# Kernel tuning notes

Measured on AMD Instinct MI355X. Metric: run time of the kernel, lower is better.

Reference implementation:

```python
import jax, jax.numpy as jnp
import numpy as np

N = 20000
E = 80000
D = 1024


def setup_inputs() -> dict:
    key = jax.random.key(0)
    ks = jax.random.split(key, 12)
    s1 = 1.0 / np.sqrt(2 * D)
    s2 = 1.0 / np.sqrt(D)
    return {
        "x": jax.random.normal(ks[0], (N, D), dtype=jnp.float32),
        "edge_index": jax.random.randint(ks[1], (2, E), 0, N, dtype=jnp.int64),
        "edge_attr": jax.random.normal(ks[2], (E, D), dtype=jnp.float32),
        "W1a": jax.random.uniform(ks[3], (2 * D, D), jnp.float32, -s1, s1),
        "b1a": jax.random.uniform(ks[4], (D,), jnp.float32, -s1, s1),
        "W1b": jax.random.uniform(ks[5], (D, D), jnp.float32, -s2, s2),
        "b1b": jax.random.uniform(ks[6], (D,), jnp.float32, -s2, s2),
        "W2a": jax.random.uniform(ks[7], (2 * D, D), jnp.float32, -s1, s1),
        "b2a": jax.random.uniform(ks[8], (D,), jnp.float32, -s1, s1),
        "W2b": jax.random.uniform(ks[9], (D, D), jnp.float32, -s2, s2),
        "b2b": jax.random.uniform(ks[10], (D,), jnp.float32, -s2, s2),
    }


def reference(x, edge_index, edge_attr, W1a, b1a, W1b, b1b, W2a, b2a, W2b, b2b):
    row, col = edge_index[0], edge_index[1]
    # gather source node features, concat edge features: [E, 2D]
    h = jnp.concatenate([x[row], edge_attr], axis=1)
    # node_mlp_1: Lin(2D,D) -> ReLU -> Lin(D,D)
    h = jax.nn.relu(h @ W1a + b1a) @ W1b + b1b  # [E, D]
    # scatter_mean over destination nodes (dim_size = N); empty segments -> 0
    sums = jax.ops.segment_sum(h, col, num_segments=N)  # [N, D]
    counts = jax.ops.segment_sum(jnp.ones((h.shape[0], 1), h.dtype), col, num_segments=N)
    mean = sums / jnp.maximum(counts, 1.0)
    # (scatter_max is computed in the torch code but its result is unused)
    out = jnp.concatenate([x, mean], axis=1)  # [N, 2D]
    # node_mlp_2
    return jax.nn.relu(out @ W2a + b2a) @ W2b + b2b  # [N, D]
```

## Files before the change

kernel.cpp:

```cpp
#include <hip/hip_runtime.h>
#include <stdint.h>

#define NN 20000
#define NE 80000
#define DD 1024

typedef __bf16 bf16x8 __attribute__((ext_vector_type(8)));
typedef float f32x4 __attribute__((ext_vector_type(4)));
typedef unsigned short u16;
typedef unsigned int u32;

__device__ __forceinline__ float bf2f(u16 v) { return __uint_as_float(((u32)v) << 16); }
__device__ __forceinline__ u16 f2bf(float f) { return (u16)((__float_as_uint(f) + 0x8000u) >> 16); }

__device__ __forceinline__ void lds_dma16(const u16* g, u16* l) {
  __builtin_amdgcn_global_load_lds((const __attribute__((address_space(1))) u32*)g,
                                   (__attribute__((address_space(3))) u32*)l, 16, 0, 0);
}

__global__ void detect_stride_k(const int* __restrict__ ei, int* flag) {
  if (threadIdx.x == 0) {
    int nz = 0;
    for (int i = 1; i < 128; i += 2) nz |= ei[i];
    *flag = (nz == 0) ? 2 : 1;
  }
}

__global__ void transpose_cvt_k(const float* __restrict__ in, u16* __restrict__ out) {
  __shared__ float tile[32][33];
  int bx = blockIdx.x * 32, by = blockIdx.y * 32;
  int tx = threadIdx.x & 31, ty = threadIdx.x >> 5;
#pragma unroll
  for (int s = 0; s < 4; s++)
    tile[ty + s * 8][tx] = in[(size_t)(by + ty + s * 8) * DD + bx + tx];
  __syncthreads();
#pragma unroll
  for (int s = 0; s < 4; s++)
    out[(size_t)(bx + ty + s * 8) * DD + by + tx] = f2bf(tile[tx][ty + s * 8]);
}

__global__ void cvt_bf16_k(const float4* __restrict__ in, ushort4* __restrict__ out, int n4) {
  int i = blockIdx.x * 256 + threadIdx.x;
  if (i < n4) {
    float4 f = in[i];
    ushort4 o;
    o.x = f2bf(f.x); o.y = f2bf(f.y); o.z = f2bf(f.z); o.w = f2bf(f.w);
    out[i] = o;
  }
}

__global__ void count_edges_k(const int* __restrict__ ei, const int* __restrict__ sflag,
                              int* __restrict__ cnt) {
  int e = blockIdx.x * 256 + threadIdx.x;
  if (e < NE) {
    int s = *sflag;
    atomicAdd(&cnt[ei[(size_t)s * (NE + e)]], 1);
  }
}

__global__ __launch_bounds__(1024) void scan_k(const int* __restrict__ cnt,
                                               int* __restrict__ rowptr, int* __restrict__ ofs) {
  __shared__ int part[1024];
  int t = threadIdx.x;
  int base = t * 20;
  int loc[20];
  int s = 0;
#pragma unroll
  for (int i = 0; i < 20; i++) {
    int v = (base + i < NN) ? cnt[base + i] : 0;
    loc[i] = s; s += v;
  }
  part[t] = s;
  __syncthreads();
  for (int d = 1; d < 1024; d <<= 1) {
    int v = (t >= d) ? part[t - d] : 0;
    __syncthreads();
    part[t] += v;
    __syncthreads();
  }
  int excl = (t > 0) ? part[t - 1] : 0;
#pragma unroll
  for (int i = 0; i < 20; i++)
    if (base + i < NN) { rowptr[base + i] = excl + loc[i]; ofs[base + i] = excl + loc[i]; }
  if (t == 1023) rowptr[NN] = part[1023];
}

__global__ void scatter_k(const int* __restrict__ ei, const int* __restrict__ sflag,
                          int* __restrict__ ofs, int* __restrict__ perm) {
  int e = blockIdx.x * 256 + threadIdx.x;
  if (e < NE) {
    int s = *sflag;
    int c = ei[(size_t)s * (NE + e)];
    perm[atomicAdd(&ofs[c], 1)] = e;
  }
}

__global__ void seg_mean_k(const u16* __restrict__ h, const int* __restrict__ rowptr,
                           const int* __restrict__ perm, u16* __restrict__ sbar) {
  int n = blockIdx.x, t = threadIdx.x;
  int beg = rowptr[n], end = rowptr[n + 1];
  float a0 = 0, a1 = 0, a2 = 0, a3 = 0;
  for (int i = beg; i < end; i++) {
    int e = perm[i];
    ushort4 v = *(const ushort4*)(h + (size_t)e * DD + t * 4);
    a0 += bf2f(v.x); a1 += bf2f(v.y); a2 += bf2f(v.z); a3 += bf2f(v.w);
  }
  float inv = (end > beg) ? 1.0f / (float)(end - beg) : 0.0f;
  ushort4 o;
  o.x = f2bf(a0 * inv); o.y = f2bf(a1 * inv); o.z = f2bf(a2 * inv); o.w = f2bf(a3 * inv);
  *(ushort4*)(sbar + (size_t)n * DD + t * 4) = o;
}

template <int EPI, int NSRC>
__global__ __launch_bounds__(256) void gemm_k(
    const u16* __restrict__ A0, const u16* __restrict__ A1,
    const u16* __restrict__ B0, const u16* __restrict__ B1, int M,
    const float* __restrict__ bias, float* __restrict__ Cout, u16* __restrict__ Cbf,
    const u16* __restrict__ Pg, u16* __restrict__ Hout,
    const int* __restrict__ eidx, const int* __restrict__ sflag,
    const int* __restrict__ cnt) {
  __shared__ __align__(16) u16 As[2][128 * 32];
  __shared__ __align__(16) u16 Bs[2][128 * 32];

  const int tid = threadIdx.x;
  const int lane = tid & 63;
  const int wv = tid >> 6;
  const int wm = wv >> 1, wn = wv & 1;

  const int nwg = gridDim.x;
  const int cpx = nwg >> 3;
  const int bid = blockIdx.x;
  const int l = (bid & 7) * cpx + (bid >> 3);
  const int nblk = l & 7, mblk = l >> 3;

  const int lrow = lane & 15, kq = lane >> 4;

  int ss = 1;
  if constexpr (EPI == 1) ss = *sflag;

  size_t a_goff[2], b_goff[2];
  int lseg[2];
#pragma unroll
  for (int r = 0; r < 2; r++) {
    int p = (wv * 2 + r) * 64 + lane;
    int row = p >> 2, c = p & 3;
    int kc = c ^ ((row >> 1) & 3);
    a_goff[r] = (size_t)min(mblk * 128 + row, M - 1) * DD + kc * 8;
    b_goff[r] = (size_t)(nblk * 128 + row) * DD + kc * 8;
    lseg[r] = (wv * 2 + r) * 512;
  }

  int a_fo[4], b_fo[4];
#pragma unroll
  for (int i = 0; i < 4; i++) {
    int m = wm * 64 + i * 16 + lrow;
    a_fo[i] = (m * 4 + (kq ^ ((m >> 1) & 3))) * 8;
    int n = wn * 64 + i * 16 + lrow;
    b_fo[i] = (n * 4 + (kq ^ ((n >> 1) & 3))) * 8;
  }

  f32x4 acc[4][4] = {};

  const int NK = NSRC * (DD / 32);

  auto stage = [&](int b, int step) {
    const u16* Ag = A0;
    const u16* Bg = B0;
    if constexpr (NSRC == 2) {
      if (step >= DD / 32) { Ag = A1; Bg = B1; }
    }
    size_t ko = (size_t)(step & (DD / 32 - 1)) * 32;
#pragma unroll
    for (int r = 0; r < 2; r++) {
      lds_dma16(Ag + a_goff[r] + ko, &As[b][lseg[r]]);
      lds_dma16(Bg + b_goff[r] + ko, &Bs[b][lseg[r]]);
    }
  };

  stage(0, 0);
  __syncthreads();

  int cur = 0;
  for (int step = 0; step < NK; step++) {
    if (step + 1 < NK) stage(cur ^ 1, step + 1);
    bf16x8 af[4], bf[4];
#pragma unroll
    for (int i = 0; i < 4; i++) {
      af[i] = *(const bf16x8*)&As[cur][a_fo[i]];
      bf[i] = *(const bf16x8*)&Bs[cur][b_fo[i]];
    }
#pragma unroll
    for (int i = 0; i < 4; i++)
#pragma unroll
      for (int j = 0; j < 4; j++)
        acc[i][j] = __builtin_amdgcn_mfma_f32_16x16x32_bf16(af[i], bf[j], acc[i][j], 0, 0, 0);
    __syncthreads();
    cur ^= 1;
  }

#pragma unroll
  for (int i = 0; i < 4; i++) {
#pragma unroll
    for (int r = 0; r < 4; r++) {
      int grow = mblk * 128 + wm * 64 + i * 16 + kq * 4 + r;
      if (grow >= M) continue;
      int erow = 0;
      if constexpr (EPI == 1) erow = eidx[(size_t)ss * grow];
#pragma unroll
      for (int j = 0; j < 4; j++) {
        int gcol = nblk * 128 + wn * 64 + j * 16 + lrow;
        float v = acc[i][j][r];
        if constexpr (EPI == 0) {
          Cout[(size_t)grow * DD + gcol] = v + bias[gcol];
        } else if constexpr (EPI == 1) {
          float z = fmaxf(v + bf2f(Pg[(size_t)erow * DD + gcol]), 0.0f);
          Hout[(size_t)grow * DD + gcol] = f2bf(z);
        } else if constexpr (EPI == 2) {
          float b = (cnt[grow] > 0) ? bias[gcol] : 0.0f;
          Cbf[(size_t)grow * DD + gcol] = f2bf(v + b);
        } else if constexpr (EPI == 3) {
          Cbf[(size_t)grow * DD + gcol] = f2bf(fmaxf(v + bias[gcol], 0.0f));
        } else {
          Cbf[(size_t)grow * DD + gcol] = f2bf(v + bias[gcol]);
        }
      }
    }
  }
}

extern "C" void kernel_launch(void* const* d_in, const int* in_sizes, int n_in,
                              void* d_out, int out_size, void* d_ws, size_t ws_size,
                              hipStream_t stream) {
  const float* x   = (const float*)d_in[0];
  const int*   ei  = (const int*)d_in[1];
  const float* ea  = (const float*)d_in[2];
  const float* W1a = (const float*)d_in[3];
  const float* b1a = (const float*)d_in[4];
  const float* W1b = (const float*)d_in[5];
  const float* b1b = (const float*)d_in[6];
  const float* W2a = (const float*)d_in[7];
  const float* b2a = (const float*)d_in[8];
  const float* W2b = (const float*)d_in[9];
  const float* b2b = (const float*)d_in[10];
  float* out = (float*)d_out;

  char* ws = (char*)d_ws;
  size_t off = 0;
  const size_t WSZ = (size_t)DD * DD;
  u16* W1aT_t = (u16*)(ws + off); off += WSZ * 2;
  u16* W1aT_b = (u16*)(ws + off); off += WSZ * 2;
  u16* W1bT   = (u16*)(ws + off); off += WSZ * 2;
  u16* W2aT_t = (u16*)(ws + off); off += WSZ * 2;
  u16* W2aT_b = (u16*)(ws + off); off += WSZ * 2;
  u16* W2bT   = (u16*)(ws + off); off += WSZ * 2;
  u16* xb   = (u16*)(ws + off); off += (size_t)NN * DD * 2;
  u16* eb   = (u16*)(ws + off); off += (size_t)NE * DD * 2;
  u16* bufP = (u16*)(ws + off); off += (size_t)NN * DD * 2;
  u16* bufM = (u16*)(ws + off); off += (size_t)NN * DD * 2;
  u16* h    = (u16*)(ws + off); off += (size_t)NE * DD * 2;
  int* cnt    = (int*)(ws + off); off += (size_t)NN * 4;
  int* rowptr = (int*)(ws + off); off += (size_t)(NN + 1) * 4;
  int* ofs    = (int*)(ws + off); off += (size_t)NN * 4;
  int* perm   = (int*)(ws + off); off += (size_t)NE * 4;
  int* sflag  = (int*)(ws + off); off += 256;
  if (ws_size < off) return;

  dim3 tb(256);
  dim3 tg(32, 32);
  transpose_cvt_k<<<tg, tb, 0, stream>>>(W1a, W1aT_t);
  transpose_cvt_k<<<tg, tb, 0, stream>>>(W1a + WSZ, W1aT_b);
  transpose_cvt_k<<<tg, tb, 0, stream>>>(W1b, W1bT);
  transpose_cvt_k<<<tg, tb, 0, stream>>>(W2a, W2aT_t);
  transpose_cvt_k<<<tg, tb, 0, stream>>>(W2a + WSZ, W2aT_b);
  transpose_cvt_k<<<tg, tb, 0, stream>>>(W2b, W2bT);

  cvt_bf16_k<<<NN * DD / 4 / 256, tb, 0, stream>>>((const float4*)x, (ushort4*)xb, NN * DD / 4);
  cvt_bf16_k<<<NE * DD / 4 / 256, tb, 0, stream>>>((const float4*)ea, (ushort4*)eb, NE * DD / 4);

  detect_stride_k<<<1, 64, 0, stream>>>(ei, sflag);
  hipMemsetAsync(cnt, 0, (size_t)NN * 4, stream);
  count_edges_k<<<(NE + 255) / 256, tb, 0, stream>>>(ei, sflag, cnt);
  scan_k<<<1, 1024, 0, stream>>>(cnt, rowptr, ofs);
  scatter_k<<<(NE + 255) / 256, tb, 0, stream>>>(ei, sflag, ofs, perm);

  const int nmbN = (NN + 127) / 128;
  const int nmbE = NE / 128;
  dim3 gN(8 * nmbN);
  dim3 gE(8 * nmbE);

  gemm_k<4, 1><<<gN, tb, 0, stream>>>(xb, nullptr, W1aT_t, nullptr, NN,
                                      b1a, nullptr, bufP, nullptr, nullptr,
                                      nullptr, nullptr, nullptr);
  gemm_k<1, 1><<<gE, tb, 0, stream>>>(eb, nullptr, W1aT_b, nullptr, NE,
                                      nullptr, nullptr, nullptr, bufP, h,
                                      ei, sflag, nullptr);
  seg_mean_k<<<NN, tb, 0, stream>>>(h, rowptr, perm, bufP);
  gemm_k<2, 1><<<gN, tb, 0, stream>>>(bufP, nullptr, W1bT, nullptr, NN,
                                      b1b, nullptr, bufM, nullptr, nullptr,
                                      nullptr, nullptr, cnt);
  gemm_k<3, 2><<<gN, tb, 0, stream>>>(xb, bufM, W2aT_t, W2aT_b, NN,
                                      b2a, nullptr, bufP, nullptr, nullptr,
                                      nullptr, nullptr, nullptr);
  gemm_k<0, 1><<<gN, tb, 0, stream>>>(bufP, nullptr, W2bT, nullptr, NN,
                                      b2b, out, nullptr, nullptr, nullptr,
                                      nullptr, nullptr, nullptr);
}
```

Measured before the change: 1.275 ms.

## Triple-buffer GEMM LDS staging with explicit vmcnt waits and MFMA priority

Replaces the double-buffered LDS pipeline in the bf16 MFMA GEMM with a three-stage ring. Loads are issued three K-steps ahead, and explicit s_waitcnt vmcnt counts plus raw s_barrier replace the full __syncthreads drain, so more global-to-LDS DMA stays in flight while MFMAs run. s_setprio is raised around the MFMA block, and launch bounds ask for 3 waves per SIMD. The cost is 50% more LDS per block, which could reduce occupancy. The hand-counted vmcnt values must match exactly four loads per stage, which is fragile.

```diff
diff --git a/kernel.cpp b/kernel.cpp
--- a/kernel.cpp
+++ b/kernel.cpp
@@ -112,15 +112,15 @@
 }
 
 template <int EPI, int NSRC>
-__global__ __launch_bounds__(256) void gemm_k(
+__global__ __launch_bounds__(256, 3) void gemm_k(
     const u16* __restrict__ A0, const u16* __restrict__ A1,
     const u16* __restrict__ B0, const u16* __restrict__ B1, int M,
     const float* __restrict__ bias, float* __restrict__ Cout, u16* __restrict__ Cbf,
     const u16* __restrict__ Pg, u16* __restrict__ Hout,
     const int* __restrict__ eidx, const int* __restrict__ sflag,
     const int* __restrict__ cnt) {
-  __shared__ __align__(16) u16 As[2][128 * 32];
-  __shared__ __align__(16) u16 Bs[2][128 * 32];
+  __shared__ __align__(16) u16 As[3][128 * 32];
+  __shared__ __align__(16) u16 Bs[3][128 * 32];
 
   const int tid = threadIdx.x;
   const int lane = tid & 63;
@@ -136,7 +136,10 @@
   const int lrow = lane & 15, kq = lane >> 4;
 
   int ss = 1;
-  if constexpr (EPI == 1) ss = *sflag;
+  if constexpr (EPI == 1) {
+    ss = *sflag;
+    asm volatile("s_waitcnt vmcnt(0)" ::: "memory");
+  }
 
   size_t a_goff[2], b_goff[2];
   int lseg[2];
@@ -177,26 +180,51 @@
     }
   };
 
-  stage(0, 0);
-  __syncthreads();
-
-  int cur = 0;
-  for (int step = 0; step < NK; step++) {
-    if (step + 1 < NK) stage(cur ^ 1, step + 1);
+  auto compute = [&](int cb) {
     bf16x8 af[4], bf[4];
 #pragma unroll
     for (int i = 0; i < 4; i++) {
-      af[i] = *(const bf16x8*)&As[cur][a_fo[i]];
-      bf[i] = *(const bf16x8*)&Bs[cur][b_fo[i]];
+      af[i] = *(const bf16x8*)&As[cb][a_fo[i]];
+      bf[i] = *(const bf16x8*)&Bs[cb][b_fo[i]];
     }
+    __builtin_amdgcn_s_setprio(1);
 #pragma unroll
     for (int i = 0; i < 4; i++)
 #pragma unroll
       for (int j = 0; j < 4; j++)
         acc[i][j] = __builtin_amdgcn_mfma_f32_16x16x32_bf16(af[i], bf[j], acc[i][j], 0, 0, 0);
-    __syncthreads();
-    cur ^= 1;
-  }
+    __builtin_amdgcn_s_setprio(0);
+  };
+
+  stage(0, 0);
+  stage(1, 1);
+  stage(2, 2);
+
+  int cur = 0;
+  for (int t = 0; t + 3 < NK; ++t) {
+    asm volatile("s_waitcnt vmcnt(8)" ::: "memory");
+    __builtin_amdgcn_s_barrier();
+    asm volatile("" ::: "memory");
+    compute(cur);
+    asm volatile("" ::: "memory");
+    __builtin_amdgcn_s_barrier();
+    stage(cur, t + 3);
+    cur = (cur == 2) ? 0 : cur + 1;
+  }
+  asm volatile("s_waitcnt vmcnt(8)" ::: "memory");
+  __builtin_amdgcn_s_barrier();
+  asm volatile("" ::: "memory");
+  compute(cur);
+  cur = (cur == 2) ? 0 : cur + 1;
+  asm volatile("s_waitcnt vmcnt(4)" ::: "memory");
+  __builtin_amdgcn_s_barrier();
+  asm volatile("" ::: "memory");
+  compute(cur);
+  cur = (cur == 2) ? 0 : cur + 1;
+  asm volatile("s_waitcnt vmcnt(0)" ::: "memory");
+  __builtin_amdgcn_s_barrier();
+  asm volatile("" ::: "memory");
+  compute(cur);
 
 #pragma unroll
   for (int i = 0; i < 4; i++) {
```

After: 1.226 ms. 3.8% less time.
